# Performance work log

Hardware: AMD Instinct MI355X
Metric: run time of the kernel (lower is better)

Reference implementation:

```python
import jax, jax.numpy as jnp
import numpy as np
from jax import lax

D_MODEL = 512
N_LAYERS = 12
D_STATE = 16
D_INNER = 2 * D_MODEL          # expand=2
DT_RANK = D_MODEL // 16        # 32
D_CONV = 4
L = 361                        # 19x19 Go board
B = 64


def silu(v):
    return v * jax.nn.sigmoid(v)


def setup_inputs() -> dict:
    key = jax.random.key(0)
    ks = jax.random.split(key, 24)
    s = 0.02
    inp = {
        "x": jax.random.normal(ks[0], (B, 17, 19, 19), dtype=jnp.float32),
        "conv1_w": jax.random.normal(ks[1], (D_MODEL // 4, 17, 3, 3)) * s,
        "conv1_b": jnp.zeros((D_MODEL // 4,)),
        "conv2_w": jax.random.normal(ks[2], (D_MODEL, D_MODEL // 4, 1, 1)) * s,
        "conv2_b": jnp.zeros((D_MODEL,)),
        "spatial_link": jax.random.normal(ks[3], (L, D_MODEL)) * s,
        # stacked per-layer Mamba parameters (leading dim = N_LAYERS)
        "in_proj_w": jax.random.normal(ks[4], (N_LAYERS, 2 * D_INNER, D_MODEL)) * s,
        "conv1d_w": jax.random.normal(ks[5], (N_LAYERS, D_INNER, D_CONV)) * 0.1,
        "conv1d_b": jnp.zeros((N_LAYERS, D_INNER)),
        "x_proj_w": jax.random.normal(ks[6], (N_LAYERS, DT_RANK + 2 * D_STATE, D_INNER)) * s,
        "dt_proj_w": jax.random.normal(ks[7], (N_LAYERS, D_INNER, DT_RANK)) * 0.1,
        "dt_proj_b": jax.random.uniform(ks[8], (N_LAYERS, D_INNER), minval=-4.0, maxval=-2.0),
        "A_log": jnp.broadcast_to(jnp.log(jnp.arange(1.0, D_STATE + 1.0)), (N_LAYERS, D_INNER, D_STATE)) * jnp.ones((N_LAYERS, D_INNER, 1)),
        "D_skip": jnp.ones((N_LAYERS, D_INNER)),
        "out_proj_w": jax.random.normal(ks[9], (N_LAYERS, D_MODEL, D_INNER)) * s,
        "ln_g": jnp.ones((D_MODEL,)),
        "ln_b": jnp.zeros((D_MODEL,)),
        "policy_w": jax.random.normal(ks[10], (362, D_MODEL)) * s,
        "policy_b": jnp.zeros((362,)),
        "value_w": jax.random.normal(ks[11], (1, D_MODEL)) * s,
        "value_b": jnp.zeros((1,)),
    }
    return inp


def _mamba_block(u, p):
    """One Mamba block. u: [B, L, d_model]; p: per-layer params."""
    ipw, cw, cb, xpw, dpw, dpb, alog, dsk, opw = p
    Lh = u.shape[1]
    xz = jnp.einsum('bld,ed->ble', u, ipw)           # [B,L,2*d_inner]
    xc, z = jnp.split(xz, 2, axis=-1)
    # depthwise causal conv1d (kernel 4, left pad 3)
    xp = jnp.pad(xc, ((0, 0), (D_CONV - 1, 0), (0, 0)))
    xc = sum(xp[:, k:k + Lh, :] * cw[:, k] for k in range(D_CONV)) + cb
    xc = silu(xc)
    dbc = jnp.einsum('bld,ed->ble', xc, xpw)          # [B,L,dt_rank+2N]
    dt_r = dbc[..., :DT_RANK]
    Bc = dbc[..., DT_RANK:DT_RANK + D_STATE]
    Cc = dbc[..., DT_RANK + D_STATE:]
    dt = jax.nn.softplus(jnp.einsum('blr,dr->bld', dt_r, dpw) + dpb)  # [B,L,d_inner]
    A = -jnp.exp(alog)                                # [d_inner, N]

    def step(h, xs_t):
        dt_t, B_t, C_t, u_t = xs_t                    # [B,d_inner],[B,N],[B,N],[B,d_inner]
        dA = jnp.exp(dt_t[:, :, None] * A)            # [B,d_inner,N]
        h = dA * h + (dt_t * u_t)[:, :, None] * B_t[:, None, :]
        y = jnp.einsum('bdn,bn->bd', h, C_t)
        return h, y

    h0 = jnp.zeros((u.shape[0], D_INNER, D_STATE), dtype=u.dtype)
    xs = (dt.transpose(1, 0, 2), Bc.transpose(1, 0, 2),
          Cc.transpose(1, 0, 2), xc.transpose(1, 0, 2))
    _, ys = lax.scan(step, h0, xs)                    # ys: [L,B,d_inner]
    y = ys.transpose(1, 0, 2) + xc * dsk
    y = y * silu(z)
    return jnp.einsum('bld,ed->ble', y, opw)


def reference(x, conv1_w, conv1_b, conv2_w, conv2_b, spatial_link,
              in_proj_w, conv1d_w, conv1d_b, x_proj_w, dt_proj_w, dt_proj_b,
              A_log, D_skip, out_proj_w, ln_g, ln_b,
              policy_w, policy_b, value_w, value_b):
    dn = ('NCHW', 'OIHW', 'NCHW')
    h = lax.conv_general_dilated(x, conv1_w, (1, 1), 'SAME', dimension_numbers=dn)
    h = silu(h + conv1_b[None, :, None, None])
    h = lax.conv_general_dilated(h, conv2_w, (1, 1), 'SAME', dimension_numbers=dn)
    h = h + conv2_b[None, :, None, None]
    b = h.shape[0]
    u = h.reshape(b, D_MODEL, L).transpose(0, 2, 1) + spatial_link  # [B,L,d_model]

    def layer(carry, p):
        return carry + _mamba_block(carry, p), None

    u, _ = lax.scan(layer, u, (in_proj_w, conv1d_w, conv1d_b, x_proj_w,
                               dt_proj_w, dt_proj_b, A_log, D_skip, out_proj_w))

    mu = u.mean(-1, keepdims=True)
    var = ((u - mu) ** 2).mean(-1, keepdims=True)
    un = (u - mu) / jnp.sqrt(var + 1e-5) * ln_g + ln_b
    xg = un.mean(axis=1)                               # [B,d_model]
    policy = xg @ policy_w.T + policy_b                # [B,362]
    value = jnp.tanh(xg @ value_w.T + value_b)         # [B,1]
    return policy, value
```

## Files before the change

### kernel.cpp

```cpp
#include <hip/hip_runtime.h>
#include <hip/hip_bf16.h>
#include <cstdint>

typedef unsigned int  uint32;
typedef unsigned short u16;
typedef __attribute__((ext_vector_type(8))) __bf16  bf16x8;
typedef __attribute__((ext_vector_type(4))) float   f32x4;
typedef __attribute__((ext_vector_type(4))) uint32  u32x4;

constexpr int BB = 64;
constexpr int LL = 361;
constexpr int DM = 512;
constexpr int DI = 1024;
constexpr int MM = BB * LL;
constexpr int POL_OUT = BB * 362;

constexpr size_t SCRATCH_BYTES = 560ull * 1024 * 1024;
__device__ __attribute__((aligned(256))) char g_scratch[SCRATCH_BYTES];

__device__ __forceinline__ uint32 bf_rne(float x) {
  uint32 u = __float_as_uint(x);
  return (u + 0x7FFFu + ((u >> 16) & 1u)) >> 16;
}

template<int BN, bool RES>
__global__ __launch_bounds__(256, 2) void gemm_hilo(
    const float* __restrict__ A, const u16* __restrict__ Whi,
    const u16* __restrict__ Wlo, float* __restrict__ C,
    int M, int K, int ldc)
{
  constexpr int BM = 128, BK = 64;
  __shared__ u16 sAh[BM * BK], sAl[BM * BK], sWh[BN * BK], sWl[BN * BK];
  const int tid = threadIdx.x;
  const int m0 = blockIdx.x * BM;
  const int n0 = blockIdx.y * BN;
  const int wave = tid >> 6, lane = tid & 63;
  const int wm = (wave >> 1) * 64;
  const int wn = (wave & 1) * (BN / 2);
  constexpr int FM = 4, FN = BN / 32;
  f32x4 acc[FM][FN];
#pragma unroll
  for (int i = 0; i < FM; ++i)
#pragma unroll
    for (int j = 0; j < FN; ++j) acc[i][j] = f32x4{0.f, 0.f, 0.f, 0.f};
  const int lr = lane & 15, lq = lane >> 4;
  constexpr int ASPT = BM / 32;
  constexpr int WSPT = BN / 32;

  for (int k0 = 0; k0 < K; k0 += BK) {
    __syncthreads();
#pragma unroll
    for (int i = 0; i < ASPT; ++i) {
      int slot = tid * ASPT + i;
      int r = slot >> 3, s = slot & 7;
      int gm = m0 + r;
      f32x4 v0 = {0.f, 0.f, 0.f, 0.f}, v1 = {0.f, 0.f, 0.f, 0.f};
      if (gm < M) {
        const float* p = A + (size_t)gm * K + (k0 + s * 8);
        v0 = *(const f32x4*)p;
        v1 = *(const f32x4*)(p + 4);
      }
      u32x4 hv, lv;
#pragma unroll
      for (int q = 0; q < 4; ++q) {
        float x0 = (q < 2) ? v0[q * 2] : v1[(q - 2) * 2];
        float x1 = (q < 2) ? v0[q * 2 + 1] : v1[(q - 2) * 2 + 1];
        uint32 b0 = __float_as_uint(x0), b1 = __float_as_uint(x1);
        hv[q] = (b0 >> 16) | (b1 & 0xFFFF0000u);
        float r0 = x0 - __uint_as_float(b0 & 0xFFFF0000u);
        float r1 = x1 - __uint_as_float(b1 & 0xFFFF0000u);
        lv[q] = bf_rne(r0) | (bf_rne(r1) << 16);
      }
      int off = r * 128 + ((s ^ (r & 7)) << 4);
      *(u32x4*)((char*)sAh + off) = hv;
      *(u32x4*)((char*)sAl + off) = lv;
    }
#pragma unroll
    for (int i = 0; i < WSPT; ++i) {
      int slot = tid * WSPT + i;
      int r = slot >> 3, s = slot & 7;
      size_t g = (size_t)(n0 + r) * K + (k0 + s * 8);
      int off = r * 128 + ((s ^ (r & 7)) << 4);
      *(u32x4*)((char*)sWh + off) = *(const u32x4*)(Whi + g);
      *(u32x4*)((char*)sWl + off) = *(const u32x4*)(Wlo + g);
    }
    __syncthreads();
#pragma unroll
    for (int kk = 0; kk < 2; ++kk) {
      bf16x8 ah[FM], al[FM], bh[FN], bl[FN];
#pragma unroll
      for (int f = 0; f < FM; ++f) {
        int row = wm + f * 16 + lr;
        int off = row * 128 + (((kk * 4 + lq) ^ (row & 7)) << 4);
        ah[f] = *(const bf16x8*)((const char*)sAh + off);
        al[f] = *(const bf16x8*)((const char*)sAl + off);
      }
#pragma unroll
      for (int f = 0; f < FN; ++f) {
        int row = wn + f * 16 + lr;
        int off = row * 128 + (((kk * 4 + lq) ^ (row & 7)) << 4);
        bh[f] = *(const bf16x8*)((const char*)sWh + off);
        bl[f] = *(const bf16x8*)((const char*)sWl + off);
      }
#pragma unroll
      for (int i = 0; i < FM; ++i)
#pragma unroll
        for (int j = 0; j < FN; ++j) {
          acc[i][j] = __builtin_amdgcn_mfma_f32_16x16x32_bf16(ah[i], bh[j], acc[i][j], 0, 0, 0);
          acc[i][j] = __builtin_amdgcn_mfma_f32_16x16x32_bf16(ah[i], bl[j], acc[i][j], 0, 0, 0);
          acc[i][j] = __builtin_amdgcn_mfma_f32_16x16x32_bf16(al[i], bh[j], acc[i][j], 0, 0, 0);
        }
    }
  }
#pragma unroll
  for (int i = 0; i < FM; ++i)
#pragma unroll
    for (int j = 0; j < FN; ++j) {
      int col = n0 + wn + j * 16 + lr;
#pragma unroll
      for (int q = 0; q < 4; ++q) {
        int row = m0 + wm + i * 16 + lq * 4 + q;
        if (row < M) {
          size_t idx = (size_t)row * ldc + col;
          float v = acc[i][j][q];
          if (RES) C[idx] += v; else C[idx] = v;
        }
      }
    }
}

__global__ void wconv_kernel(const float* __restrict__ w, u16* __restrict__ hi,
                             u16* __restrict__ lo, int n4) {
  int i = blockIdx.x * 256 + threadIdx.x;
  if (i >= n4) return;
  f32x4 v = *(const f32x4*)&w[(size_t)i * 4];
  uint32 hp[2], lp[2];
#pragma unroll
  for (int q = 0; q < 2; ++q) {
    float x0 = v[q * 2], x1 = v[q * 2 + 1];
    uint32 b0 = __float_as_uint(x0), b1 = __float_as_uint(x1);
    hp[q] = (b0 >> 16) | (b1 & 0xFFFF0000u);
    float r0 = x0 - __uint_as_float(b0 & 0xFFFF0000u);
    float r1 = x1 - __uint_as_float(b1 & 0xFFFF0000u);
    lp[q] = bf_rne(r0) | (bf_rne(r1) << 16);
  }
  ((uint32*)hi)[(size_t)i * 2]     = hp[0];
  ((uint32*)hi)[(size_t)i * 2 + 1] = hp[1];
  ((uint32*)lo)[(size_t)i * 2]     = lp[0];
  ((uint32*)lo)[(size_t)i * 2 + 1] = lp[1];
}

__global__ void w2t_kernel(const float* __restrict__ w2, float* __restrict__ w2t) {
  int i = blockIdx.x * 256 + threadIdx.x;
  if (i < 512 * 128) { int co = i >> 7, ci = i & 127; w2t[ci * 512 + co] = w2[i]; }
}

__global__ void pwt_kernel(const float* __restrict__ pw, float* __restrict__ pwt) {
  int i = blockIdx.x * 256 + threadIdx.x;
  if (i < 362 * 512) { int j = i / 512, dd = i & 511; pwt[dd * 362 + j] = pw[i]; }
}

__global__ void conv1_kernel(const float* __restrict__ x, const float* __restrict__ w,
                             const float* __restrict__ bias, float* __restrict__ h1) {
  __shared__ float xs[17 * 361];
  __shared__ float wls[16 * 153];
  const int b = blockIdx.x, cg = blockIdx.y * 16;
  const int tid = threadIdx.x;
  for (int i = tid; i < 17 * 361; i += 384) xs[i] = x[(size_t)b * 17 * 361 + i];
  for (int i = tid; i < 16 * 153; i += 384) wls[i] = w[(size_t)cg * 153 + i];
  __syncthreads();
  if (tid >= 361) return;
  const int py = tid / 19, px = tid % 19;
  float* outp = h1 + ((size_t)b * 361 + tid) * 128 + cg;
  for (int c = 0; c < 16; ++c) {
    float acc = bias[cg + c];
    const float* wc = wls + c * 153;
    for (int ci = 0; ci < 17; ++ci) {
      const float* xi = xs + ci * 361;
      const float* wi = wc + ci * 9;
#pragma unroll
      for (int ky = 0; ky < 3; ++ky) {
        int iy = py + ky - 1;
        if (iy < 0 || iy >= 19) continue;
#pragma unroll
        for (int kx = 0; kx < 3; ++kx) {
          int ix = px + kx - 1;
          if (ix < 0 || ix >= 19) continue;
          acc += xi[iy * 19 + ix] * wi[ky * 3 + kx];
        }
      }
    }
    outp[c] = acc / (1.f + __expf(-acc));
  }
}

__global__ void conv2_kernel(const float* __restrict__ h1, const float* __restrict__ w2t,
                             const float* __restrict__ b2, const float* __restrict__ sl,
                             float* __restrict__ u) {
  __shared__ float hs[8][128];
  const int b = blockIdx.x, l0 = blockIdx.y * 8;
  const int nl = min(8, 361 - l0);
  const int tid = threadIdx.x;
  for (int i = tid; i < nl * 128; i += 512)
    hs[i >> 7][i & 127] = h1[((size_t)b * 361 + l0 + (i >> 7)) * 128 + (i & 127)];
  __syncthreads();
  float acc[8];
#pragma unroll
  for (int j = 0; j < 8; ++j) acc[j] = 0.f;
  for (int ci = 0; ci < 128; ++ci) {
    float wv = w2t[ci * 512 + tid];
#pragma unroll
    for (int j = 0; j < 8; ++j) acc[j] += hs[j][ci] * wv;
  }
  float bb = b2[tid];
  for (int j = 0; j < nl; ++j) {
    int l = l0 + j;
    u[((size_t)b * 361 + l) * 512 + tid] = acc[j] + bb + sl[(size_t)l * 512 + tid];
  }
}

__global__ void conv1d_kernel(const float* __restrict__ xz, const float* __restrict__ cw,
                              const float* __restrict__ cb, float* __restrict__ xca) {
  const int b = blockIdx.x, l0 = blockIdx.y * 32;
  const int d = threadIdx.x * 4;
  float w[4][4], bias[4];
#pragma unroll
  for (int j = 0; j < 4; ++j) {
#pragma unroll
    for (int k = 0; k < 4; ++k) w[j][k] = cw[(d + j) * 4 + k];
    bias[j] = cb[d + j];
  }
  f32x4 h0 = {0, 0, 0, 0}, h1v = {0, 0, 0, 0}, h2v = {0, 0, 0, 0};
  if (l0 >= 3) h0  = *(const f32x4*)&xz[((size_t)b * 361 + l0 - 3) * 2048 + d];
  if (l0 >= 2) h1v = *(const f32x4*)&xz[((size_t)b * 361 + l0 - 2) * 2048 + d];
  if (l0 >= 1) h2v = *(const f32x4*)&xz[((size_t)b * 361 + l0 - 1) * 2048 + d];
  const int nl = min(32, 361 - l0);
  for (int t = 0; t < nl; ++t) {
    const int l = l0 + t;
    f32x4 cur = *(const f32x4*)&xz[((size_t)b * 361 + l) * 2048 + d];
    f32x4 o;
#pragma unroll
    for (int j = 0; j < 4; ++j) {
      float v = h0[j] * w[j][0] + h1v[j] * w[j][1] + h2v[j] * w[j][2] + cur[j] * w[j][3] + bias[j];
      o[j] = v / (1.f + __expf(-v));
    }
    *(f32x4*)&xca[((size_t)b * 361 + l) * 1024 + d] = o;
    h0 = h1v; h1v = h2v; h2v = cur;
  }
}

__global__ void dt_kernel(const float* __restrict__ dbc, const float* __restrict__ dpw,
                          const float* __restrict__ dpb, float* __restrict__ dty) {
  __shared__ float dbs[32][32];
  const int m0 = blockIdx.x * 32, d0 = blockIdx.y * 256;
  const int tid = threadIdx.x;
  {
    int r = tid >> 3, c = (tid & 7) * 4;
    *(f32x4*)&dbs[r][c] = *(const f32x4*)&dbc[(size_t)(m0 + r) * 64 + c];
  }
  __syncthreads();
  float wreg[32];
  const float* wp = dpw + (size_t)(d0 + tid) * 32;
#pragma unroll
  for (int q = 0; q < 8; ++q) {
    f32x4 v = *(const f32x4*)&wp[q * 4];
    wreg[q * 4] = v[0]; wreg[q * 4 + 1] = v[1]; wreg[q * 4 + 2] = v[2]; wreg[q * 4 + 3] = v[3];
  }
  const float bias = dpb[d0 + tid];
  for (int m = 0; m < 32; ++m) {
    float acc = bias;
#pragma unroll
    for (int r = 0; r < 32; ++r) acc += dbs[m][r] * wreg[r];
    float sp = fmaxf(acc, 0.f) + log1pf(__expf(-fabsf(acc)));
    dty[(size_t)(m0 + m) * 1024 + d0 + tid] = sp;
  }
}

__global__ void scan_kernel(const float* __restrict__ dbc, const float* __restrict__ xca,
                            const float* __restrict__ xz, const float* __restrict__ alog,
                            const float* __restrict__ dsk, float* dty) {
  const int b = blockIdx.x;
  const int d = blockIdx.y * 256 + threadIdx.x;
  float Ax[16], h[16];
#pragma unroll
  for (int n = 0; n < 16; ++n) { Ax[n] = -__expf(alog[(size_t)d * 16 + n]); h[n] = 0.f; }
  const float dval = dsk[d];
  const size_t mb = (size_t)b * 361;
  for (int t = 0; t < 361; ++t) {
    const size_t m = mb + t;
    const float dtv = dty[m * 1024 + d];
    const float uv  = xca[m * 1024 + d];
    const float zv  = xz[m * 2048 + 1024 + d];
    const float* bcp = dbc + m * 64 + 32;
    const float du = dtv * uv;
    float yv = 0.f;
#pragma unroll
    for (int n = 0; n < 16; ++n) {
      float dA = __expf(dtv * Ax[n]);
      h[n] = dA * h[n] + du * bcp[n];
      yv += h[n] * bcp[16 + n];
    }
    yv += uv * dval;
    float sz = zv / (1.f + __expf(-zv));
    dty[m * 1024 + d] = yv * sz;
  }
}

__global__ void ln_stats_kernel(const float* __restrict__ u, float* __restrict__ muv,
                                float* __restrict__ rsd) {
  const int m = blockIdx.x * 4 + (threadIdx.x >> 6);
  const int lane = threadIdx.x & 63;
  const float* row = u + (size_t)m * 512;
  float s = 0.f, s2 = 0.f;
#pragma unroll
  for (int i = 0; i < 2; ++i) {
    f32x4 v = *(const f32x4*)&row[(lane + i * 64) * 4];
    s  += v[0] + v[1] + v[2] + v[3];
    s2 += v[0] * v[0] + v[1] * v[1] + v[2] * v[2] + v[3] * v[3];
  }
#pragma unroll
  for (int o = 32; o > 0; o >>= 1) { s += __shfl_down(s, o); s2 += __shfl_down(s2, o); }
  if (lane == 0) {
    float mean = s * (1.f / 512.f);
    float var = s2 * (1.f / 512.f) - mean * mean;
    muv[m] = mean;
    rsd[m] = rsqrtf(var + 1e-5f);
  }
}

__global__ void xg_kernel(const float* __restrict__ u, const float* __restrict__ muv,
                          const float* __restrict__ rsd, const float* __restrict__ g,
                          const float* __restrict__ bta, float* __restrict__ xg) {
  const int b = blockIdx.x, dd = threadIdx.x;
  float acc = 0.f;
  const size_t mb = (size_t)b * 361;
  for (int l = 0; l < 361; ++l) {
    const size_t m = mb + l;
    acc += (u[m * 512 + dd] - muv[m]) * rsd[m];
  }
  xg[(size_t)b * 512 + dd] = g[dd] * acc * (1.f / 361.f) + bta[dd];
}

__global__ void head_kernel(const float* __restrict__ xg, const float* __restrict__ pwt,
                            const float* __restrict__ pb, const float* __restrict__ vw,
                            const float* __restrict__ vb, float* __restrict__ out) {
  __shared__ float xs[512];
  const int b = blockIdx.x, tid = threadIdx.x;
  xs[tid] = xg[(size_t)b * 512 + tid];
  __syncthreads();
  if (tid < 362) {
    float acc = pb[tid];
    for (int dd = 0; dd < 512; ++dd) acc += xs[dd] * pwt[dd * 362 + tid];
    out[(size_t)b * 362 + tid] = acc;
  } else if (tid == 384) {
    float acc = vb[0];
    for (int dd = 0; dd < 512; ++dd) acc += xs[dd] * vw[dd];
    out[POL_OUT + b] = tanhf(acc);
  }
}

extern "C" void kernel_launch(void* const* d_in, const int* in_sizes, int n_in,
                              void* d_out, int out_size, void* d_ws, size_t ws_size,
                              hipStream_t stream) {
  const float* x     = (const float*)d_in[0];
  const float* c1w   = (const float*)d_in[1];
  const float* c1b   = (const float*)d_in[2];
  const float* c2w   = (const float*)d_in[3];
  const float* c2b   = (const float*)d_in[4];
  const float* slink = (const float*)d_in[5];
  const float* ipw   = (const float*)d_in[6];
  const float* cdw   = (const float*)d_in[7];
  const float* cdb   = (const float*)d_in[8];
  const float* xpw   = (const float*)d_in[9];
  const float* dpw   = (const float*)d_in[10];
  const float* dpb   = (const float*)d_in[11];
  const float* alog  = (const float*)d_in[12];
  const float* dskp  = (const float*)d_in[13];
  const float* opw   = (const float*)d_in[14];
  const float* lng   = (const float*)d_in[15];
  const float* lnb   = (const float*)d_in[16];
  const float* pw    = (const float*)d_in[17];
  const float* pb    = (const float*)d_in[18];
  const float* vw    = (const float*)d_in[19];
  const float* vb    = (const float*)d_in[20];
  float* out = (float*)d_out;
  (void)in_sizes; (void)n_in; (void)out_size; (void)d_ws; (void)ws_size;

  char* base = nullptr;
  hipGetSymbolAddress((void**)&base, HIP_SYMBOL(g_scratch));
  size_t off = 0;
  auto carve = [&](size_t bytes) -> char* {
    char* p = base + off;
    off += (bytes + 255) & ~(size_t)255;
    return p;
  };
  float* u    = (float*)carve((size_t)MM * DM * 4);
  float* xz   = (float*)carve((size_t)MM * 2 * DI * 4);
  float* xca  = (float*)carve((size_t)MM * DI * 4);
  float* dty  = (float*)carve((size_t)MM * DI * 4);
  float* dbc  = (float*)carve((size_t)MM * 64 * 4);
  float* h1   = (float*)carve((size_t)BB * LL * 128 * 4);
  float* w2t  = (float*)carve(512 * 128 * 4);
  float* pwt  = (float*)carve(512 * 362 * 4);
  float* muv  = (float*)carve((size_t)MM * 4);
  float* rsd  = (float*)carve((size_t)MM * 4);
  float* xg   = (float*)carve((size_t)BB * DM * 4);
  u16* wih = (u16*)carve((size_t)12 * 2048 * 512 * 2);
  u16* wil = (u16*)carve((size_t)12 * 2048 * 512 * 2);
  u16* wxh = (u16*)carve((size_t)12 * 64 * 1024 * 2);
  u16* wxl = (u16*)carve((size_t)12 * 64 * 1024 * 2);
  u16* woh = (u16*)carve((size_t)12 * 512 * 1024 * 2);
  u16* wol = (u16*)carve((size_t)12 * 512 * 1024 * 2);

  wconv_kernel<<<dim3(12288), dim3(256), 0, stream>>>(ipw, wih, wil, 3145728);
  wconv_kernel<<<dim3(768),   dim3(256), 0, stream>>>(xpw, wxh, wxl, 196608);
  wconv_kernel<<<dim3(6144),  dim3(256), 0, stream>>>(opw, woh, wol, 1572864);
  w2t_kernel<<<dim3(256), dim3(256), 0, stream>>>(c2w, w2t);
  pwt_kernel<<<dim3(724), dim3(256), 0, stream>>>(pw, pwt);

  conv1_kernel<<<dim3(64, 8),  dim3(384), 0, stream>>>(x, c1w, c1b, h1);
  conv2_kernel<<<dim3(64, 46), dim3(512), 0, stream>>>(h1, w2t, c2b, slink, u);

  for (int layer = 0; layer < 12; ++layer) {
    gemm_hilo<128, false><<<dim3(181, 16), dim3(256), 0, stream>>>(
        u, wih + (size_t)layer * 1048576, wil + (size_t)layer * 1048576, xz, MM, 512, 2048);
    conv1d_kernel<<<dim3(64, 12), dim3(256), 0, stream>>>(
        xz, cdw + (size_t)layer * 4096, cdb + (size_t)layer * 1024, xca);
    gemm_hilo<64, false><<<dim3(181, 1), dim3(256), 0, stream>>>(
        xca, wxh + (size_t)layer * 65536, wxl + (size_t)layer * 65536, dbc, MM, 1024, 64);
    dt_kernel<<<dim3(722, 4), dim3(256), 0, stream>>>(
        dbc, dpw + (size_t)layer * 32768, dpb + (size_t)layer * 1024, dty);
    scan_kernel<<<dim3(64, 4), dim3(256), 0, stream>>>(
        dbc, xca, xz, alog + (size_t)layer * 16384, dskp + (size_t)layer * 1024, dty);
    gemm_hilo<128, true><<<dim3(181, 4), dim3(256), 0, stream>>>(
        dty, woh + (size_t)layer * 524288, wol + (size_t)layer * 524288, u, MM, 1024, 512);
  }

  ln_stats_kernel<<<dim3(5776), dim3(256), 0, stream>>>(u, muv, rsd);
  xg_kernel<<<dim3(64), dim3(512), 0, stream>>>(u, muv, rsd, lng, lnb, xg);
  head_kernel<<<dim3(64), dim3(512), 0, stream>>>(xg, pwt, pb, vw, vb, out);
}
```

Baseline: 10.49 ms.

## Store activations as pre-split bf16 hi/lo planes and stage GEMM tiles via direct LDS loads

Producers (conv2, conv1d, scan, out-proj epilogue) now write activations as separate bf16 hi and lo planes instead of fp32. The GEMMs then load A tiles straight into LDS with global_load_lds, so the per-tile fp32 load and hi/lo split inside the GEMM main loop goes away. The x_proj GEMM switches to 64x64 tiles to get more blocks. The split buffers are padded to MP rows so tile loads past M read allocated memory. In exchange, producer kernels do the split work, extra hi/lo buffers are written, and scan reconstructs its input from two planes.

After: 9.205 ms. -12.3%, faster.

```diff
diff --git a/kernel.cpp b/kernel.cpp
--- a/kernel.cpp
+++ b/kernel.cpp
@@ -7,83 +7,82 @@
 typedef __attribute__((ext_vector_type(8))) __bf16  bf16x8;
 typedef __attribute__((ext_vector_type(4))) float   f32x4;
 typedef __attribute__((ext_vector_type(4))) uint32  u32x4;
+typedef __attribute__((ext_vector_type(4))) u16     u16x4;
 
 constexpr int BB = 64;
 constexpr int LL = 361;
 constexpr int DM = 512;
 constexpr int DI = 1024;
 constexpr int MM = BB * LL;
+constexpr int MP = 23168;
 constexpr int POL_OUT = BB * 362;
 
-constexpr size_t SCRATCH_BYTES = 560ull * 1024 * 1024;
+constexpr size_t SCRATCH_BYTES = 700ull * 1024 * 1024;
 __device__ __attribute__((aligned(256))) char g_scratch[SCRATCH_BYTES];
 
 __device__ __forceinline__ uint32 bf_rne(float x) {
   uint32 u = __float_as_uint(x);
   return (u + 0x7FFFu + ((u >> 16) & 1u)) >> 16;
 }
-
-template<int BN, bool RES>
-__global__ __launch_bounds__(256, 2) void gemm_hilo(
-    const float* __restrict__ A, const u16* __restrict__ Whi,
-    const u16* __restrict__ Wlo, float* __restrict__ C,
+__device__ __forceinline__ void split2(float v, u16& h, u16& l) {
+  uint32 b = __float_as_uint(v);
+  h = (u16)(b >> 16);
+  l = (u16)bf_rne(v - __uint_as_float(b & 0xFFFF0000u));
+}
+__device__ __forceinline__ float join2(u16 h, u16 l) {
+  return __uint_as_float((uint32)h << 16) + __uint_as_float((uint32)l << 16);
+}
+
+template<int ROWS>
+__device__ __forceinline__ void stage_swz(const u16* __restrict__ plane, int row0,
+                                          int K, int k0, u16* lds,
+                                          int wave, int lane) {
+  const int lrow = lane >> 3, lslot = lane & 7;
+  constexpr int RPW = ROWS / 4;
+#pragma unroll
+  for (int i = 0; i < RPW / 8; ++i) {
+    int rr = wave * RPW + i * 8 + lrow;
+    int sg = lslot ^ (rr & 7);
+    const u16* src = plane + (size_t)(row0 + rr) * K + k0 + sg * 8;
+    u16* dst = lds + (wave * RPW + i * 8) * 64;
+    __builtin_amdgcn_global_load_lds(
+        (const __attribute__((address_space(1))) void*)src,
+        (__attribute__((address_space(3))) void*)dst, 16, 0, 0);
+  }
+}
+
+template<int BM, int BN, bool RES, bool WPL>
+__global__ __launch_bounds__(256, 2) void gemm_pl(
+    const u16* __restrict__ Ahi, const u16* __restrict__ Alo,
+    const u16* __restrict__ Whi, const u16* __restrict__ Wlo,
+    float* __restrict__ C, u16* __restrict__ Chi, u16* __restrict__ Clo,
     int M, int K, int ldc)
 {
-  constexpr int BM = 128, BK = 64;
-  __shared__ u16 sAh[BM * BK], sAl[BM * BK], sWh[BN * BK], sWl[BN * BK];
+  constexpr int BK = 64;
+  __shared__ __attribute__((aligned(16))) u16 sAh[BM * 64];
+  __shared__ __attribute__((aligned(16))) u16 sAl[BM * 64];
+  __shared__ __attribute__((aligned(16))) u16 sWh[BN * 64];
+  __shared__ __attribute__((aligned(16))) u16 sWl[BN * 64];
   const int tid = threadIdx.x;
   const int m0 = blockIdx.x * BM;
   const int n0 = blockIdx.y * BN;
   const int wave = tid >> 6, lane = tid & 63;
-  const int wm = (wave >> 1) * 64;
+  const int wm = (wave >> 1) * (BM / 2);
   const int wn = (wave & 1) * (BN / 2);
-  constexpr int FM = 4, FN = BN / 32;
+  constexpr int FM = BM / 32, FN = BN / 32;
   f32x4 acc[FM][FN];
 #pragma unroll
   for (int i = 0; i < FM; ++i)
 #pragma unroll
     for (int j = 0; j < FN; ++j) acc[i][j] = f32x4{0.f, 0.f, 0.f, 0.f};
   const int lr = lane & 15, lq = lane >> 4;
-  constexpr int ASPT = BM / 32;
-  constexpr int WSPT = BN / 32;
 
   for (int k0 = 0; k0 < K; k0 += BK) {
     __syncthreads();
-#pragma unroll
-    for (int i = 0; i < ASPT; ++i) {
-      int slot = tid * ASPT + i;
-      int r = slot >> 3, s = slot & 7;
-      int gm = m0 + r;
-      f32x4 v0 = {0.f, 0.f, 0.f, 0.f}, v1 = {0.f, 0.f, 0.f, 0.f};
-      if (gm < M) {
-        const float* p = A + (size_t)gm * K + (k0 + s * 8);
-        v0 = *(const f32x4*)p;
-        v1 = *(const f32x4*)(p + 4);
-      }
-      u32x4 hv, lv;
-#pragma unroll
-      for (int q = 0; q < 4; ++q) {
-        float x0 = (q < 2) ? v0[q * 2] : v1[(q - 2) * 2];
-        float x1 = (q < 2) ? v0[q * 2 + 1] : v1[(q - 2) * 2 + 1];
-        uint32 b0 = __float_as_uint(x0), b1 = __float_as_uint(x1);
-        hv[q] = (b0 >> 16) | (b1 & 0xFFFF0000u);
-        float r0 = x0 - __uint_as_float(b0 & 0xFFFF0000u);
-        float r1 = x1 - __uint_as_float(b1 & 0xFFFF0000u);
-        lv[q] = bf_rne(r0) | (bf_rne(r1) << 16);
-      }
-      int off = r * 128 + ((s ^ (r & 7)) << 4);
-      *(u32x4*)((char*)sAh + off) = hv;
-      *(u32x4*)((char*)sAl + off) = lv;
-    }
-#pragma unroll
-    for (int i = 0; i < WSPT; ++i) {
-      int slot = tid * WSPT + i;
-      int r = slot >> 3, s = slot & 7;
-      size_t g = (size_t)(n0 + r) * K + (k0 + s * 8);
-      int off = r * 128 + ((s ^ (r & 7)) << 4);
-      *(u32x4*)((char*)sWh + off) = *(const u32x4*)(Whi + g);
-      *(u32x4*)((char*)sWl + off) = *(const u32x4*)(Wlo + g);
-    }
+    stage_swz<BM>(Ahi, m0, K, k0, sAh, wave, lane);
+    stage_swz<BM>(Alo, m0, K, k0, sAl, wave, lane);
+    stage_swz<BN>(Whi, n0, K, k0, sWh, wave, lane);
+    stage_swz<BN>(Wlo, n0, K, k0, sWl, wave, lane);
     __syncthreads();
 #pragma unroll
     for (int kk = 0; kk < 2; ++kk) {
@@ -123,7 +122,9 @@
         if (row < M) {
           size_t idx = (size_t)row * ldc + col;
           float v = acc[i][j][q];
-          if (RES) C[idx] += v; else C[idx] = v;
+          if (RES) v += C[idx];
+          C[idx] = v;
+          if (WPL) { u16 h, l; split2(v, h, l); Chi[idx] = h; Clo[idx] = l; }
         }
       }
     }
@@ -134,20 +135,11 @@
   int i = blockIdx.x * 256 + threadIdx.x;
   if (i >= n4) return;
   f32x4 v = *(const f32x4*)&w[(size_t)i * 4];
-  uint32 hp[2], lp[2];
-#pragma unroll
-  for (int q = 0; q < 2; ++q) {
-    float x0 = v[q * 2], x1 = v[q * 2 + 1];
-    uint32 b0 = __float_as_uint(x0), b1 = __float_as_uint(x1);
-    hp[q] = (b0 >> 16) | (b1 & 0xFFFF0000u);
-    float r0 = x0 - __uint_as_float(b0 & 0xFFFF0000u);
-    float r1 = x1 - __uint_as_float(b1 & 0xFFFF0000u);
-    lp[q] = bf_rne(r0) | (bf_rne(r1) << 16);
-  }
-  ((uint32*)hi)[(size_t)i * 2]     = hp[0];
-  ((uint32*)hi)[(size_t)i * 2 + 1] = hp[1];
-  ((uint32*)lo)[(size_t)i * 2]     = lp[0];
-  ((uint32*)lo)[(size_t)i * 2 + 1] = lp[1];
+  u16x4 hv, lv;
+#pragma unroll
+  for (int q = 0; q < 4; ++q) { u16 h, l; split2(v[q], h, l); hv[q] = h; lv[q] = l; }
+  *(u16x4*)&hi[(size_t)i * 4] = hv;
+  *(u16x4*)&lo[(size_t)i * 4] = lv;
 }
 
 __global__ void w2t_kernel(const float* __restrict__ w2, float* __restrict__ w2t) {
@@ -196,7 +188,8 @@
 
 __global__ void conv2_kernel(const float* __restrict__ h1, const float* __restrict__ w2t,
                              const float* __restrict__ b2, const float* __restrict__ sl,
-                             float* __restrict__ u) {
+                             float* __restrict__ u, u16* __restrict__ uhi,
+                             u16* __restrict__ ulo) {
   __shared__ float hs[8][128];
   const int b = blockIdx.x, l0 = blockIdx.y * 8;
   const int nl = min(8, 361 - l0);
@@ -215,12 +208,17 @@
   float bb = b2[tid];
   for (int j = 0; j < nl; ++j) {
     int l = l0 + j;
-    u[((size_t)b * 361 + l) * 512 + tid] = acc[j] + bb + sl[(size_t)l * 512 + tid];
+    size_t idx = ((size_t)b * 361 + l) * 512 + tid;
+    float v = acc[j] + bb + sl[(size_t)l * 512 + tid];
+    u[idx] = v;
+    u16 h, lo; split2(v, h, lo);
+    uhi[idx] = h; ulo[idx] = lo;
   }
 }
 
 __global__ void conv1d_kernel(const float* __restrict__ xz, const float* __restrict__ cw,
-                              const float* __restrict__ cb, float* __restrict__ xca) {
+                              const float* __restrict__ cb, u16* __restrict__ xchi,
+                              u16* __restrict__ xclo) {
   const int b = blockIdx.x, l0 = blockIdx.y * 32;
   const int d = threadIdx.x * 4;
   float w[4][4], bias[4];
@@ -238,13 +236,16 @@
   for (int t = 0; t < nl; ++t) {
     const int l = l0 + t;
     f32x4 cur = *(const f32x4*)&xz[((size_t)b * 361 + l) * 2048 + d];
-    f32x4 o;
+    u16x4 hv, lv;
 #pragma unroll
     for (int j = 0; j < 4; ++j) {
       float v = h0[j] * w[j][0] + h1v[j] * w[j][1] + h2v[j] * w[j][2] + cur[j] * w[j][3] + bias[j];
-      o[j] = v / (1.f + __expf(-v));
+      v = v / (1.f + __expf(-v));
+      u16 h, lo; split2(v, h, lo); hv[j] = h; lv[j] = lo;
     }
-    *(f32x4*)&xca[((size_t)b * 361 + l) * 1024 + d] = o;
+    size_t idx = ((size_t)b * 361 + l) * 1024 + d;
+    *(u16x4*)&xchi[idx] = hv;
+    *(u16x4*)&xclo[idx] = lv;
     h0 = h1v; h1v = h2v; h2v = cur;
   }
 }
@@ -276,9 +277,11 @@
   }
 }
 
-__global__ void scan_kernel(const float* __restrict__ dbc, const float* __restrict__ xca,
-                            const float* __restrict__ xz, const float* __restrict__ alog,
-                            const float* __restrict__ dsk, float* dty) {
+__global__ void scan_kernel(const float* __restrict__ dbc, const u16* __restrict__ xchi,
+                            const u16* __restrict__ xclo, const float* __restrict__ xz,
+                            const float* __restrict__ alog, const float* __restrict__ dsk,
+                            const float* __restrict__ dty, u16* __restrict__ yhi,
+                            u16* __restrict__ ylo) {
   const int b = blockIdx.x;
   const int d = blockIdx.y * 256 + threadIdx.x;
   float Ax[16], h[16];
@@ -289,7 +292,7 @@
   for (int t = 0; t < 361; ++t) {
     const size_t m = mb + t;
     const float dtv = dty[m * 1024 + d];
-    const float uv  = xca[m * 1024 + d];
+    const float uv  = join2(xchi[m * 1024 + d], xclo[m * 1024 + d]);
     const float zv  = xz[m * 2048 + 1024 + d];
     const float* bcp = dbc + m * 64 + 32;
     const float du = dtv * uv;
@@ -302,7 +305,10 @@
     }
     yv += uv * dval;
     float sz = zv / (1.f + __expf(-zv));
-    dty[m * 1024 + d] = yv * sz;
+    float yo = yv * sz;
+    u16 hh, ll; split2(yo, hh, ll);
+    yhi[m * 1024 + d] = hh;
+    ylo[m * 1024 + d] = ll;
   }
 }
 
@@ -396,7 +402,6 @@
   };
   float* u    = (float*)carve((size_t)MM * DM * 4);
   float* xz   = (float*)carve((size_t)MM * 2 * DI * 4);
-  float* xca  = (float*)carve((size_t)MM * DI * 4);
   float* dty  = (float*)carve((size_t)MM * DI * 4);
   float* dbc  = (float*)carve((size_t)MM * 64 * 4);
   float* h1   = (float*)carve((size_t)BB * LL * 128 * 4);
@@ -405,6 +410,12 @@
   float* muv  = (float*)carve((size_t)MM * 4);
   float* rsd  = (float*)carve((size_t)MM * 4);
   float* xg   = (float*)carve((size_t)BB * DM * 4);
+  u16* uhi  = (u16*)carve((size_t)MP * DM * 2);
+  u16* ulo  = (u16*)carve((size_t)MP * DM * 2);
+  u16* xchi = (u16*)carve((size_t)MP * DI * 2);
+  u16* xclo = (u16*)carve((size_t)MP * DI * 2);
+  u16* yhi  = (u16*)carve((size_t)MP * DI * 2);
+  u16* ylo  = (u16*)carve((size_t)MP * DI * 2);
   u16* wih = (u16*)carve((size_t)12 * 2048 * 512 * 2);
   u16* wil = (u16*)carve((size_t)12 * 2048 * 512 * 2);
   u16* wxh = (u16*)carve((size_t)12 * 64 * 1024 * 2);
@@ -419,21 +430,25 @@
   pwt_kernel<<<dim3(724), dim3(256), 0, stream>>>(pw, pwt);
 
   conv1_kernel<<<dim3(64, 8),  dim3(384), 0, stream>>>(x, c1w, c1b, h1);
-  conv2_kernel<<<dim3(64, 46), dim3(512), 0, stream>>>(h1, w2t, c2b, slink, u);
+  conv2_kernel<<<dim3(64, 46), dim3(512), 0, stream>>>(h1, w2t, c2b, slink, u, uhi, ulo);
 
   for (int layer = 0; layer < 12; ++layer) {
-    gemm_hilo<128, false><<<dim3(181, 16), dim3(256), 0, stream>>>(
-        u, wih + (size_t)layer * 1048576, wil + (size_t)layer * 1048576, xz, MM, 512, 2048);
+    gemm_pl<128, 128, false, false><<<dim3(181, 16), dim3(256), 0, stream>>>(
+        uhi, ulo, wih + (size_t)layer * 1048576, wil + (size_t)layer * 1048576,
+        xz, nullptr, nullptr, MM, 512, 2048);
     conv1d_kernel<<<dim3(64, 12), dim3(256), 0, stream>>>(
-        xz, cdw + (size_t)layer * 4096, cdb + (size_t)layer * 1024, xca);
-    gemm_hilo<64, false><<<dim3(181, 1), dim3(256), 0, stream>>>(
-        xca, wxh + (size_t)layer * 65536, wxl + (size_t)layer * 65536, dbc, MM, 1024, 64);
+        xz, cdw + (size_t)layer * 4096, cdb + (size_t)layer * 1024, xchi, xclo);
+    gemm_pl<64, 64, false, false><<<dim3(362, 1), dim3(256), 0, stream>>>(
+        xchi, xclo, wxh + (size_t)layer * 65536, wxl + (size_t)layer * 65536,
+        dbc, nullptr, nullptr, MM, 1024, 64);
     dt_kernel<<<dim3(722, 4), dim3(256), 0, stream>>>(
         dbc, dpw + (size_t)layer * 32768, dpb + (size_t)layer * 1024, dty);
     scan_kernel<<<dim3(64, 4), dim3(256), 0, stream>>>(
-        dbc, xca, xz, alog + (size_t)layer * 16384, dskp + (size_t)layer * 1024, dty);
-    gemm_hilo<128, true><<<dim3(181, 4), dim3(256), 0, stream>>>(
-        dty, woh + (size_t)layer * 524288, wol + (size_t)layer * 524288, u, MM, 1024, 512);
+        dbc, xchi, xclo, xz, alog + (size_t)layer * 16384, dskp + (size_t)layer * 1024,
+        dty, yhi, ylo);
+    gemm_pl<128, 128, true, true><<<dim3(181, 4), dim3(256), 0, stream>>>(
+        yhi, ylo, woh + (size_t)layer * 524288, wol + (size_t)layer * 524288,
+        u, uhi, ulo, MM, 1024, 512);
   }
 
   ln_stats_kernel<<<dim3(5776), dim3(256), 0, stream>>>(u, muv, rsd);
```
